# Optimization experiments

Hardware: AMD Instinct MI355X
Metric: run time of the kernel (lower is better)

The kernel has to match this reference:

```python
import jax, jax.numpy as jnp
import numpy as np

N_NODES = 100000
N_EDGES = 1600000
F_IN = 128
OUT = 32
PERIODS = 12


def setup_inputs() -> dict:
    key = jax.random.key(0)
    ks = jax.random.split(key, 12)
    s = 0.05
    return {
        'x': jax.random.normal(ks[0], (N_NODES, F_IN, PERIODS), jnp.float32),
        'edge_index': jax.random.randint(ks[1], (2, N_EDGES), 0, N_NODES, dtype=jnp.int64),
        'Wz': jax.random.normal(ks[2], (F_IN, OUT), jnp.float32) * s,
        'bz': jnp.zeros((OUT,), jnp.float32),
        'Lz': jax.random.normal(ks[3], (2 * OUT, OUT), jnp.float32) * s,
        'lbz': jnp.zeros((OUT,), jnp.float32),
        'Wh': jax.random.normal(ks[4], (F_IN, OUT), jnp.float32) * s,
        'bh': jnp.zeros((OUT,), jnp.float32),
        'Lh': jax.random.normal(ks[5], (2 * OUT, OUT), jnp.float32) * s,
        'lbh': jnp.zeros((OUT,), jnp.float32),
        'att': jax.random.normal(ks[6], (PERIODS,), jnp.float32),
        'Wlin': jax.random.normal(ks[7], (OUT, PERIODS), jnp.float32) * s,
        'blin': jnp.zeros((PERIODS,), jnp.float32),
    }


def _gcn_norm(edge_index, n):
    # GCNConv normalization with self loops: D^-1/2 (A+I) D^-1/2
    loop = jnp.arange(n, dtype=edge_index.dtype)
    row = jnp.concatenate([edge_index[0], loop])  # sources
    col = jnp.concatenate([edge_index[1], loop])  # targets
    deg = jax.ops.segment_sum(jnp.ones(row.shape[0], jnp.float32), col, num_segments=n)
    dis = jnp.where(deg > 0, jax.lax.rsqrt(deg), 0.0)
    return row, col, dis[row] * dis[col]


def reference(x, edge_index, Wz, bz, Lz, lbz, Wh, bh, Lh, lbh, att, Wlin, blin):
    n = x.shape[0]
    row, col, norm = _gcn_norm(edge_index, n)
    probs = jax.nn.softmax(att)
    xP = jnp.transpose(x, (2, 0, 1))  # [P, N, F]
    H0 = jnp.zeros((n, OUT), x.dtype)

    def conv(xp, W, b):
        xw = xp @ W                              # [N, OUT]
        msg = xw[row] * norm[:, None]            # gather at source
        return jax.ops.segment_sum(msg, col, num_segments=n) + b

    def step(acc, inp):
        xp, p = inp
        # TGCN cell with H=0 (A3TGCN passes H=None each period)
        Z = jax.nn.sigmoid(jnp.concatenate([conv(xp, Wz, bz), H0], axis=1) @ Lz + lbz)
        Ht = jnp.tanh(jnp.concatenate([conv(xp, Wh, bh), H0], axis=1) @ Lh + lbh)
        Hp = (1.0 - Z) * Ht                      # Z*H + (1-Z)*Ht with H=0
        return acc + p * Hp, None

    acc, _ = jax.lax.scan(step, H0, (xP, probs))
    h = jax.nn.relu(acc)
    return h @ Wlin + blin
```

## Files before the change

### kernel.cpp

```cpp
#include <hip/hip_runtime.h>
#include <hip/hip_fp16.h>

#define N_NODES 100000
#define N_EDGES 1600000
#define F_IN 128
#define OUT 32
#define PERIODS 12

__global__ void k_prep(const float* __restrict__ Wz, const float* __restrict__ bz,
                       const float* __restrict__ Lz, const float* __restrict__ lbz,
                       const float* __restrict__ Wh, const float* __restrict__ bh,
                       const float* __restrict__ Lh, const float* __restrict__ lbh,
                       const float* __restrict__ att,
                       float* __restrict__ M, float* __restrict__ cc,
                       float* __restrict__ probs) {
    int t = threadIdx.x;
    for (int idx = t; idx < F_IN * 64; idx += 256) {
        int f = idx >> 6, c = idx & 63;
        const float* W = (c < 32) ? Wz : Wh;
        const float* L = (c < 32) ? Lz : Lh;
        int cj = c & 31;
        float s = 0.f;
        #pragma unroll 8
        for (int j = 0; j < 32; ++j) s += W[f * 32 + j] * L[j * 32 + cj];
        M[idx] = s;
    }
    if (t < 64) {
        int c = t & 31;
        const float* b  = (t < 32) ? bz : bh;
        const float* L  = (t < 32) ? Lz : Lh;
        const float* lb = (t < 32) ? lbz : lbh;
        float s = lb[c];
        for (int j = 0; j < 32; ++j) s += b[j] * L[j * 32 + c];
        cc[t] = s;
    }
    if (t == 0) {
        float m = att[0];
        for (int p = 1; p < PERIODS; ++p) m = fmaxf(m, att[p]);
        float e[PERIODS]; float sum = 0.f;
        for (int p = 0; p < PERIODS; ++p) { e[p] = expf(att[p] - m); sum += e[p]; }
        for (int p = 0; p < PERIODS; ++p) probs[p] = e[p] / sum;
    }
}

__global__ void k_count(const int* __restrict__ ei, int* __restrict__ cnt) {
    int e = blockIdx.x * 256 + threadIdx.x;
    if (e < N_EDGES) {
        int c = ei[N_EDGES + e];
        if ((unsigned)c < N_NODES) atomicAdd(&cnt[c], 1);
    }
}

__global__ void k_dis(const int* __restrict__ cnt, float* __restrict__ dis) {
    int i = blockIdx.x * 256 + threadIdx.x;
    if (i < N_NODES) dis[i] = rsqrtf((float)(cnt[i] + 1));
}

__global__ void k_scan1(const int* __restrict__ cnt, int* __restrict__ rp,
                        int* __restrict__ partials) {
    __shared__ int s[256];
    int t = threadIdx.x;
    int i = blockIdx.x * 256 + t;
    int v = (i < N_NODES) ? cnt[i] : 0;
    s[t] = v;
    __syncthreads();
    for (int off = 1; off < 256; off <<= 1) {
        int y = (t >= off) ? s[t - off] : 0;
        __syncthreads();
        s[t] += y;
        __syncthreads();
    }
    if (i < N_NODES) rp[i] = s[t] - v;
    if (t == 255) partials[blockIdx.x] = s[255];
}

__global__ void k_scan2(int* __restrict__ partials, int np) {
    __shared__ int s[512];
    int t = threadIdx.x;
    int v = (t < np) ? partials[t] : 0;
    s[t] = v;
    __syncthreads();
    for (int off = 1; off < 512; off <<= 1) {
        int y = (t >= off) ? s[t - off] : 0;
        __syncthreads();
        s[t] += y;
        __syncthreads();
    }
    if (t < np) partials[t] = s[t] - v;
}

__global__ void k_scan3(int* __restrict__ rp, const int* __restrict__ partials) {
    int i = blockIdx.x * 256 + threadIdx.x;
    if (i < N_NODES) rp[i] += partials[blockIdx.x];
    if (i == 0) rp[N_NODES] = N_EDGES;
}

__global__ void k_fill(const int* __restrict__ ei, const int* __restrict__ rp,
                       int* __restrict__ cursor, int* __restrict__ srcIdx) {
    int e = blockIdx.x * 256 + threadIdx.x;
    if (e < N_EDGES) {
        int c = ei[N_EDGES + e];
        int r = ei[e];
        if ((unsigned)c < N_NODES) {
            int pos = rp[c] + atomicAdd(&cursor[c], 1);
            srcIdx[pos] = r;
        }
    }
}

__global__ __launch_bounds__(256, 2) void k_proj2(const float* __restrict__ x,
                                                  const float* __restrict__ M,
                                                  __half* __restrict__ U) {
    __shared__ float sM[F_IN * 64];
    __shared__ float4 sx[16 * 48];
    int t = threadIdx.x;
    int lane = t & 63;
    int wv = t >> 6;

    {
        const float4* Mv = reinterpret_cast<const float4*>(M);
        float4* sMv = reinterpret_cast<float4*>(sM);
        #pragma unroll
        for (int i = 0; i < 8; ++i) sMv[t + 256 * i] = Mv[t + 256 * i];
    }

    int nb0 = blockIdx.x * 16;
    float acc[4][PERIODS];
    #pragma unroll
    for (int a = 0; a < 4; ++a)
        #pragma unroll
        for (int p = 0; p < PERIODS; ++p) acc[a][p] = 0.f;

    const float4* xg = reinterpret_cast<const float4*>(x) + (size_t)nb0 * 384;

    for (int kc = 0; kc < 8; ++kc) {
        __syncthreads();
        #pragma unroll
        for (int i = 0; i < 3; ++i) {
            int j = t + 256 * i;
            int node = j / 48;
            int within = j - node * 48;
            sx[j] = xg[(size_t)node * 384 + kc * 48 + within];
        }
        __syncthreads();
        #pragma unroll
        for (int f = 0; f < 16; ++f) {
            float m = sM[(kc * 16 + f) * 64 + lane];
            #pragma unroll
            for (int nn = 0; nn < 4; ++nn) {
                int base = (wv * 4 + nn) * 48 + f * 3;
                float4 xa = sx[base];
                float4 xb = sx[base + 1];
                float4 xc = sx[base + 2];
                acc[nn][0]  += xa.x * m; acc[nn][1]  += xa.y * m;
                acc[nn][2]  += xa.z * m; acc[nn][3]  += xa.w * m;
                acc[nn][4]  += xb.x * m; acc[nn][5]  += xb.y * m;
                acc[nn][6]  += xb.z * m; acc[nn][7]  += xb.w * m;
                acc[nn][8]  += xc.x * m; acc[nn][9]  += xc.y * m;
                acc[nn][10] += xc.z * m; acc[nn][11] += xc.w * m;
            }
        }
    }

    #pragma unroll
    for (int nn = 0; nn < 4; ++nn) {
        __half* un = U + (size_t)(nb0 + wv * 4 + nn) * 768;
        #pragma unroll
        for (int p = 0; p < PERIODS; ++p) un[p * 64 + lane] = __float2half(acc[nn][p]);
    }
}

__global__ void k_agg(const __half* __restrict__ U, const int* __restrict__ rp,
                      const int* __restrict__ srcIdx, const float* __restrict__ dis,
                      const float* __restrict__ cc, const float* __restrict__ probs,
                      const float* __restrict__ Wlin, const float* __restrict__ blin,
                      float* __restrict__ out) {
    int n = blockIdx.x;
    int t = threadIdx.x;
    float dn = dis[n];

    float a0, a1, a2, a3;
    {
        union { uint2 u; __half2 h[2]; } r;
        r.u = reinterpret_cast<const uint2*>(U + (size_t)n * 768)[t];
        float2 f0 = __half22float2(r.h[0]);
        float2 f1 = __half22float2(r.h[1]);
        float w = dn * dn;
        a0 = w * f0.x; a1 = w * f0.y; a2 = w * f1.x; a3 = w * f1.y;
    }
    int beg = rp[n], end = rp[n + 1];
    int e = beg;
    for (; e + 1 < end; e += 2) {
        int s0 = srcIdx[e];
        int s1 = srcIdx[e + 1];
        float w0 = dis[s0] * dn;
        float w1 = dis[s1] * dn;
        union { uint2 u; __half2 h[2]; } r0, r1;
        r0.u = reinterpret_cast<const uint2*>(U + (size_t)s0 * 768)[t];
        r1.u = reinterpret_cast<const uint2*>(U + (size_t)s1 * 768)[t];
        float2 a = __half22float2(r0.h[0]);
        float2 b = __half22float2(r0.h[1]);
        a0 += w0 * a.x; a1 += w0 * a.y; a2 += w0 * b.x; a3 += w0 * b.y;
        float2 c = __half22float2(r1.h[0]);
        float2 d = __half22float2(r1.h[1]);
        a0 += w1 * c.x; a1 += w1 * c.y; a2 += w1 * d.x; a3 += w1 * d.y;
    }
    if (e < end) {
        int s = srcIdx[e];
        float w = dis[s] * dn;
        union { uint2 u; __half2 h[2]; } r;
        r.u = reinterpret_cast<const uint2*>(U + (size_t)s * 768)[t];
        float2 f0 = __half22float2(r.h[0]);
        float2 f1 = __half22float2(r.h[1]);
        a0 += w * f0.x; a1 += w * f0.y; a2 += w * f1.x; a3 += w * f1.y;
    }

    __shared__ float sacc[768];
    __shared__ float sterm[PERIODS * 32];
    __shared__ float shf[32];
    sacc[4 * t + 0] = a0; sacc[4 * t + 1] = a1;
    sacc[4 * t + 2] = a2; sacc[4 * t + 3] = a3;
    __syncthreads();

    for (int w2 = t; w2 < PERIODS * 32; w2 += 192) {
        int p = w2 >> 5, c = w2 & 31;
        float z = sacc[p * 64 + c]      + cc[c];
        float h = sacc[p * 64 + 32 + c] + cc[32 + c];
        float zs = 1.f / (1.f + __expf(-z));
        sterm[w2] = probs[p] * (1.f - zs) * tanhf(h);
    }
    __syncthreads();

    if (t < 32) {
        float s = 0.f;
        #pragma unroll
        for (int p = 0; p < PERIODS; ++p) s += sterm[p * 32 + t];
        shf[t] = fmaxf(s, 0.f);
    }
    __syncthreads();

    if (t < PERIODS) {
        float o = blin[t];
        #pragma unroll 8
        for (int c = 0; c < OUT; ++c) o += shf[c] * Wlin[c * PERIODS + t];
        out[(size_t)n * PERIODS + t] = o;
    }
}

extern "C" void kernel_launch(void* const* d_in, const int* in_sizes, int n_in,
                              void* d_out, int out_size, void* d_ws, size_t ws_size,
                              hipStream_t stream) {
    const float* x    = (const float*)d_in[0];
    const int*   ei   = (const int*)d_in[1];
    const float* Wz   = (const float*)d_in[2];
    const float* bz   = (const float*)d_in[3];
    const float* Lz   = (const float*)d_in[4];
    const float* lbz  = (const float*)d_in[5];
    const float* Wh   = (const float*)d_in[6];
    const float* bh   = (const float*)d_in[7];
    const float* Lh   = (const float*)d_in[8];
    const float* lbh  = (const float*)d_in[9];
    const float* att  = (const float*)d_in[10];
    const float* Wlin = (const float*)d_in[11];
    const float* blin = (const float*)d_in[12];
    float* out = (float*)d_out;

    char* w = (char*)d_ws;
    size_t off = 0;
    __half* U      = (__half*)(w + off); off += (size_t)N_NODES * 768 * 2;
    float*  M      = (float*)(w + off);  off += 128 * 64 * 4;
    float*  cc     = (float*)(w + off);  off += 256;
    float*  probs  = (float*)(w + off);  off += 64;
    float*  dis    = (float*)(w + off);  off += N_NODES * 4;
    int*    cnt    = (int*)(w + off);    off += N_NODES * 4;
    int*    rp     = (int*)(w + off);    off += (N_NODES + 1) * 4 + 12;
    int*    cursor = (int*)(w + off);    off += N_NODES * 4;
    int*    parts  = (int*)(w + off);    off += 2048;
    int*    srcIdx = (int*)(w + off);    off += (size_t)N_EDGES * 4;
    (void)ws_size; (void)in_sizes; (void)n_in; (void)out_size;

    const int SCAN_BLOCKS = (N_NODES + 255) / 256;

    hipMemsetAsync(cnt, 0, N_NODES * 4, stream);
    hipMemsetAsync(cursor, 0, N_NODES * 4, stream);

    k_prep<<<1, 256, 0, stream>>>(Wz, bz, Lz, lbz, Wh, bh, Lh, lbh, att, M, cc, probs);
    k_count<<<(N_EDGES + 255) / 256, 256, 0, stream>>>(ei, cnt);
    k_dis<<<SCAN_BLOCKS, 256, 0, stream>>>(cnt, dis);
    k_scan1<<<SCAN_BLOCKS, 256, 0, stream>>>(cnt, rp, parts);
    k_scan2<<<1, 512, 0, stream>>>(parts, SCAN_BLOCKS);
    k_scan3<<<SCAN_BLOCKS, 256, 0, stream>>>(rp, parts);
    k_fill<<<(N_EDGES + 255) / 256, 256, 0, stream>>>(ei, rp, cursor, srcIdx);
    k_proj2<<<N_NODES / 16, 256, 0, stream>>>(x, M, U);
    k_agg<<<N_NODES, 192, 0, stream>>>(U, rp, srcIdx, dis, cc, probs, Wlin, blin, out);
}
```

Before: 913.0 us.

## Remap projection kernel to per-thread 4-channel by 12-period register tile

The projection kernel's thread mapping changes from each wave lane owning one output channel across four nodes to each thread owning four contiguous channels of a single node. M is now read from shared memory as float4, the x tile is padded to a stride of 49 to avoid LDS bank conflicts, and the outputs are packed into uint2 half stores. The launch bounds are raised to three blocks per CU. The goal is fewer LDS loads per FMA and higher occupancy for this memory-bound pass, at the risk of register pressure under the tighter bound. Shared memory use (about 44 KB per block) may also limit how many blocks actually fit per CU.

```diff
diff --git a/kernel.cpp b/kernel.cpp
--- a/kernel.cpp
+++ b/kernel.cpp
@@ -108,14 +108,14 @@
     }
 }
 
-__global__ __launch_bounds__(256, 2) void k_proj2(const float* __restrict__ x,
+__global__ __launch_bounds__(256, 3) void k_proj3(const float* __restrict__ x,
                                                   const float* __restrict__ M,
                                                   __half* __restrict__ U) {
     __shared__ float sM[F_IN * 64];
-    __shared__ float4 sx[16 * 48];
-    int t = threadIdx.x;
-    int lane = t & 63;
-    int wv = t >> 6;
+    __shared__ float4 sx[16 * 49];
+    int t = threadIdx.x;
+    int cidx = t & 15;
+    int node = t >> 4;
 
     {
         const float4* Mv = reinterpret_cast<const float4*>(M);
@@ -127,9 +127,9 @@
     int nb0 = blockIdx.x * 16;
     float acc[4][PERIODS];
     #pragma unroll
-    for (int a = 0; a < 4; ++a)
-        #pragma unroll
-        for (int p = 0; p < PERIODS; ++p) acc[a][p] = 0.f;
+    for (int c = 0; c < 4; ++c)
+        #pragma unroll
+        for (int p = 0; p < PERIODS; ++p) acc[c][p] = 0.f;
 
     const float4* xg = reinterpret_cast<const float4*>(x) + (size_t)nb0 * 384;
 
@@ -138,35 +138,38 @@
         #pragma unroll
         for (int i = 0; i < 3; ++i) {
             int j = t + 256 * i;
-            int node = j / 48;
-            int within = j - node * 48;
-            sx[j] = xg[(size_t)node * 384 + kc * 48 + within];
+            int nd = j / 48;
+            int wi = j - nd * 48;
+            sx[nd * 49 + wi] = xg[(size_t)nd * 384 + kc * 48 + wi];
         }
         __syncthreads();
         #pragma unroll
         for (int f = 0; f < 16; ++f) {
-            float m = sM[(kc * 16 + f) * 64 + lane];
+            float4 m4 = *reinterpret_cast<const float4*>(&sM[(kc * 16 + f) * 64 + 4 * cidx]);
+            int xb = node * 49 + f * 3;
+            float4 xv0 = sx[xb];
+            float4 xv1 = sx[xb + 1];
+            float4 xv2 = sx[xb + 2];
+            float mm[4] = {m4.x, m4.y, m4.z, m4.w};
+            float xv[PERIODS] = {xv0.x, xv0.y, xv0.z, xv0.w,
+                                 xv1.x, xv1.y, xv1.z, xv1.w,
+                                 xv2.x, xv2.y, xv2.z, xv2.w};
             #pragma unroll
-            for (int nn = 0; nn < 4; ++nn) {
-                int base = (wv * 4 + nn) * 48 + f * 3;
-                float4 xa = sx[base];
-                float4 xb = sx[base + 1];
-                float4 xc = sx[base + 2];
-                acc[nn][0]  += xa.x * m; acc[nn][1]  += xa.y * m;
-                acc[nn][2]  += xa.z * m; acc[nn][3]  += xa.w * m;
-                acc[nn][4]  += xb.x * m; acc[nn][5]  += xb.y * m;
-                acc[nn][6]  += xb.z * m; acc[nn][7]  += xb.w * m;
-                acc[nn][8]  += xc.x * m; acc[nn][9]  += xc.y * m;
-                acc[nn][10] += xc.z * m; acc[nn][11] += xc.w * m;
-            }
+            for (int c = 0; c < 4; ++c)
+                #pragma unroll
+                for (int p = 0; p < PERIODS; ++p)
+                    acc[c][p] += mm[c] * xv[p];
         }
     }
 
+    __half* un = U + (size_t)(nb0 + node) * 768 + 4 * cidx;
     #pragma unroll
-    for (int nn = 0; nn < 4; ++nn) {
-        __half* un = U + (size_t)(nb0 + wv * 4 + nn) * 768;
-        #pragma unroll
-        for (int p = 0; p < PERIODS; ++p) un[p * 64 + lane] = __float2half(acc[nn][p]);
+    for (int p = 0; p < PERIODS; ++p) {
+        __half2 h0 = __floats2half2_rn(acc[0][p], acc[1][p]);
+        __half2 h1 = __floats2half2_rn(acc[2][p], acc[3][p]);
+        union { uint2 u; __half2 h[2]; } r;
+        r.h[0] = h0; r.h[1] = h1;
+        *reinterpret_cast<uint2*>(un + p * 64) = r.u;
     }
 }
 
@@ -291,6 +294,6 @@
     k_scan2<<<1, 512, 0, stream>>>(parts, SCAN_BLOCKS);
     k_scan3<<<SCAN_BLOCKS, 256, 0, stream>>>(rp, parts);
     k_fill<<<(N_EDGES + 255) / 256, 256, 0, stream>>>(ei, rp, cursor, srcIdx);
-    k_proj2<<<N_NODES / 16, 256, 0, stream>>>(x, M, U);
+    k_proj3<<<N_NODES / 16, 256, 0, stream>>>(x, M, U);
     k_agg<<<N_NODES, 192, 0, stream>>>(U, rp, srcIdx, dis, cc, probs, Wlin, blin, out);
 }
```

New measurement: 809.3 us. -11.4%, faster.
